# Optimization experiments

Measured on AMD Instinct MI355X. Metric: run time of the kernel, lower is better.

## Reference

```python
import jax, jax.numpy as jnp
import numpy as np

EMB_DIM, TREE_DIM, OUT_DIM, VOCAB = 256, 256, 3, 10000
T, B, LEVELS = 255, 128, 8  # complete binary tree of depth 8, 128 trees per input


def _build_forest():
    # node j = T-1-heap(j): root (heap 0) is the LAST node so stack_last_h picks the root.
    heap = np.arange(T)
    depth = np.floor(np.log2(heap + 1)).astype(np.int64)  # 0..7
    node_order = np.empty(T, dtype=np.int64)
    node_order[T - 1 - heap] = (LEVELS - 1) - depth       # leaves=0, root=7
    internal = np.arange((T - 1) // 2)                     # heaps with two children
    parent = np.repeat(T - 1 - internal, 2)
    child = np.stack([T - 1 - (2 * internal + 1), T - 1 - (2 * internal + 2)], 1).reshape(-1)
    edges = np.stack([parent, child], axis=1)              # (254, 2)
    edge_order = node_order[parent]
    offs = (np.arange(B) * T)[:, None, None]
    adj = (edges[None] + offs).reshape(-1, 2)              # (B*254, 2)
    return np.tile(node_order, B), adj, np.tile(edge_order, B)


def setup_inputs() -> dict:
    key = jax.random.key(0)
    ks = jax.random.split(key, 16)
    no, adj, eo = _build_forest()
    D = TREE_DIM
    s_e = 1.0 / np.sqrt(EMB_DIM)
    s_t = 1.0 / np.sqrt(D)
    return {
        'feat_cube': jax.random.randint(ks[0], (B * T,), 0, VOCAB),
        'feat_a': jax.random.randint(ks[1], (B * T,), 0, VOCAB),
        'feat_b': jax.random.randint(ks[2], (B * T,), 0, VOCAB),
        'node_order': jnp.asarray(no),
        'adjacency_list': jnp.asarray(adj),
        'edge_order': jnp.asarray(eo),
        'num_levels': LEVELS,
        'num_trees': B,
        'emb': jax.random.normal(ks[3], (VOCAB, EMB_DIM), jnp.float32),
        'W_iou': jax.random.normal(ks[4], (3 * D, EMB_DIM), jnp.float32) * s_e,
        'b_iou': jnp.zeros((3 * D,), jnp.float32),
        'U_iou': jax.random.normal(ks[5], (3 * D, D), jnp.float32) * s_t,
        'W_f': jax.random.normal(ks[6], (D, EMB_DIM), jnp.float32) * s_e,
        'b_f': jnp.zeros((D,), jnp.float32),
        'U_f': jax.random.normal(ks[7], (D, D), jnp.float32) * s_t,
        'fc1_w': jax.random.normal(ks[8], (D // 2, D), jnp.float32) * s_t,
        'fc1_b': jnp.zeros((D // 2,), jnp.float32),
        'fc2_w': jax.random.normal(ks[9], (OUT_DIM, D // 2), jnp.float32) * (1.0 / np.sqrt(D // 2)),
        'fc2_b': jnp.zeros((OUT_DIM,), jnp.float32),
    }


def _tree_lstm(x, node_order, parents, children, edge_order, W_iou, b_iou, U_iou, W_f, b_f, U_f, num_levels):
    # Child-sum TreeLSTM, evaluated level by level (leaves first). Dense masked
    # formulation: per level we update only nodes with node_order==lvl; edge
    # contributions are masked before segment_sum (same math as the torch loop).
    N = x.shape[0]
    D = U_f.shape[0]
    x_iou = x @ W_iou.T + b_iou            # (N, 3D), precomputed once
    x_f = x @ W_f.T + b_f                  # (N, D)
    h = jnp.zeros((N, D), x.dtype)
    c = jnp.zeros((N, D), x.dtype)
    for lvl in range(num_levels):
        emask = (edge_order == lvl)[:, None].astype(x.dtype)
        ch = h[children]                   # (E, D) gather of child hidden
        cc = c[children]
        f = jax.nn.sigmoid(x_f[parents] + ch @ U_f.T)
        h_sum = jax.ops.segment_sum(ch * emask, parents, num_segments=N)
        c_sum = jax.ops.segment_sum(f * cc * emask, parents, num_segments=N)
        i, o, u = jnp.split(x_iou + h_sum @ U_iou.T, 3, axis=1)
        c_new = jax.nn.sigmoid(i) * jnp.tanh(u) + c_sum
        h_new = jax.nn.sigmoid(o) * jnp.tanh(c_new)
        nmask = (node_order == lvl)[:, None]
        h = jnp.where(nmask, h_new, h)
        c = jnp.where(nmask, c_new, c)
    return h, c


def reference(feat_cube, feat_a, feat_b, node_order, adjacency_list, edge_order,
              num_levels, num_trees, emb, W_iou, b_iou, U_iou, W_f, b_f, U_f,
              fc1_w, fc1_b, fc2_w, fc2_b):
    parents = adjacency_list[:, 0]
    children = adjacency_list[:, 1]

    def run_tree(feat):
        h, _ = _tree_lstm(emb[feat], node_order, parents, children, edge_order,
                          W_iou, b_iou, U_iou, W_f, b_f, U_f, num_levels)
        # stack_last_h: last node of each tree (= root with our labeling)
        return h.reshape(num_trees, -1, h.shape[-1])[:, -1, :]

    h_c = run_tree(feat_cube)
    h_a = run_tree(feat_a)
    h_b = run_tree(feat_b)
    # h_c (1,D) @ (h_a (D,1) @ h_b (1,D)) == (h_c . h_a) * h_b, fused einsum
    h = jnp.einsum('bi,bi,bj->bj', h_c, h_a, h_b)
    hid = jax.nn.relu(h @ fc1_w.T + fc1_b)
    logits = jax.nn.relu(hid @ fc2_w.T + fc2_b)
    return logits  # (num_trees, out_dim)
```

## Files before the change

### kernel.cpp

```cpp
#include <hip/hip_runtime.h>
#include <hip/hip_bf16.h>

typedef __hip_bfloat16 bf16;
typedef unsigned short u16;
typedef __attribute__((ext_vector_type(8))) short s8;
typedef __attribute__((ext_vector_type(4))) float f4;

#define NRUNS 3
#define NTREE 128
#define TT    255
#define DD    256
#define VPAD  10016
#define PAD   258
#define ESTR  776

__device__ __forceinline__ float bits2f(u16 b){ union{unsigned u; float f;} x; x.u = ((unsigned)b)<<16; return x.f; }
__device__ __forceinline__ u16   f2bits(float f){ bf16 h = __float2bfloat16(f); return *(u16*)&h; }
__device__ __forceinline__ float sigm(float x){ return 1.f/(1.f+__expf(-x)); }
__device__ __forceinline__ float tanh_(float x){ return 1.f - 2.f/(__expf(2.f*x)+1.f); }

__global__ void k_detect(const u16* __restrict__ raw, int* __restrict__ flag){
    int t = threadIdx.x;
    int hit = 0;
    if (t < 128){
        u16 w = raw[2*t];
        int e = (w >> 7) & 0xFF;
        hit = (e >= 100 && e <= 141) ? 1 : 0;
    }
    __shared__ int cnt;
    if (t == 0) cnt = 0;
    __syncthreads();
    atomicAdd(&cnt, hit);
    __syncthreads();
    if (t == 0) flag[0] = (cnt >= 64) ? 1 : 0;
}

__device__ __forceinline__ u16 cvt1b(const void* p, int i, int isb){
    return isb ? ((const u16*)p)[i] : f2bits(((const float*)p)[i]);
}
__device__ __forceinline__ float cvt1f(const void* p, int i, int isb){
    return isb ? bits2f(((const u16*)p)[i]) : ((const float*)p)[i];
}

#define L_EMB  (10000*256)
#define L_EMBP (VPAD*256)
#define L_WIOU (768*256)
#define L_UIOU (768*256)
#define L_WF   (256*256)
#define L_UF   (256*256)
#define L_ALL  (L_EMBP + L_WIOU + L_UIOU + L_WF + L_UF)
__global__ void k_cvtb(const void* __restrict__ s0, const void* __restrict__ s1,
                       const void* __restrict__ s2, const void* __restrict__ s3,
                       const void* __restrict__ s4,
                       u16* __restrict__ d0, u16* __restrict__ d1, u16* __restrict__ d2,
                       u16* __restrict__ d3, u16* __restrict__ d4,
                       const int* __restrict__ flag){
    int isb = flag[0];
    for (int i = blockIdx.x*blockDim.x + threadIdx.x; i < L_ALL; i += gridDim.x*blockDim.x){
        int j = i;
        if (j < L_EMBP){ d0[j] = (j < L_EMB) ? cvt1b(s0, j, isb) : (u16)0; continue; } j -= L_EMBP;
        if (j < L_WIOU){ d1[j] = cvt1b(s1, j, isb); continue; } j -= L_WIOU;
        if (j < L_UIOU){ d2[j] = cvt1b(s2, j, isb); continue; } j -= L_UIOU;
        if (j < L_WF){ d3[j] = cvt1b(s3, j, isb); continue; } j -= L_WF;
        d4[j] = cvt1b(s4, j, isb);
    }
}

#define S_BIOU 768
#define S_BF   256
#define S_F1W  (128*256)
#define S_F1B  128
#define S_F2W  (3*128)
#define S_F2B  3
#define S_ALL  (S_BIOU+S_BF+S_F1W+S_F1B+S_F2W+S_F2B)
__global__ void k_small(const void* __restrict__ s0, const void* __restrict__ s1,
                        const void* __restrict__ s2, const void* __restrict__ s3,
                        const void* __restrict__ s4, const void* __restrict__ s5,
                        float* __restrict__ d0, float* __restrict__ d1, float* __restrict__ d2,
                        float* __restrict__ d3, float* __restrict__ d4, float* __restrict__ d5,
                        const int* __restrict__ flag){
    int isb = flag[0];
    for (int i = blockIdx.x*blockDim.x + threadIdx.x; i < S_ALL; i += gridDim.x*blockDim.x){
        int j = i;
        if (j < S_BIOU){ d0[j] = cvt1f(s0, j, isb); continue; } j -= S_BIOU;
        if (j < S_BF){ d1[j] = cvt1f(s1, j, isb); continue; } j -= S_BF;
        if (j < S_F1W){ d2[j] = cvt1f(s2, j, isb); continue; } j -= S_F1W;
        if (j < S_F1B){ d3[j] = cvt1f(s3, j, isb); continue; } j -= S_F1B;
        if (j < S_F2W){ d4[j] = cvt1f(s4, j, isb); continue; } j -= S_F2W;
        d5[j] = cvt1f(s5, j, isb);
    }
}

__device__ __forceinline__ s8 ldB16(const u16* p){
    union { uint4 q; s8 v; } u;
    u.q = *(const uint4*)p;
    return u.v;
}
__device__ __forceinline__ s8 ldsA(const u16* p){
    union { unsigned w[4]; s8 v; } u;
    u.w[0] = *(const unsigned*)(p);
    u.w[1] = *(const unsigned*)(p+2);
    u.w[2] = *(const unsigned*)(p+4);
    u.w[3] = *(const unsigned*)(p+6);
    return u.v;
}
#define MFMA(acc,a,b) acc = __builtin_amdgcn_mfma_f32_16x16x32_bf16(a, b, acc, 0, 0, 0)

__global__ __launch_bounds__(512, 4)
void k_vocab2(const u16* __restrict__ embb,
              const u16* __restrict__ Wiou, const u16* __restrict__ Wfm,
              const u16* __restrict__ Ufm,  const float* __restrict__ biou_f,
              u16* __restrict__ E_iou, u16* __restrict__ E_f,
              u16* __restrict__ H0, u16* __restrict__ C0, u16* __restrict__ HU0)
{
    __shared__ u16 hs[32*PAD];
    const int t = threadIdx.x, w = t>>6, lane = t&63, ln = lane&15, q = lane>>4;
    const int r0 = blockIdx.x*32, d0 = w*32;

    const u16* Bp[8];
    #pragma unroll
    for (int g = 0; g < 4; g++)
      #pragma unroll
      for (int nc = 0; nc < 2; nc++){
        int nn = d0 + nc*16 + ln;
        Bp[g*2+nc] = (g < 3) ? (Wiou + (size_t)(g*256+nn)*DD) : (Wfm + (size_t)nn*DD);
      }
    const u16* a0p = embb + (size_t)(r0+ln)*DD;
    const u16* a1p = embb + (size_t)(r0+16+ln)*DD;
    f4 acc[8][2];
    #pragma unroll
    for (int nt = 0; nt < 8; nt++){ acc[nt][0] = (f4){0,0,0,0}; acc[nt][1] = (f4){0,0,0,0}; }
    #pragma unroll 2
    for (int ks = 0; ks < 8; ks++){
        int ko = ks*32 + q*8;
        s8 a0 = ldB16(a0p + ko);
        s8 a1 = ldB16(a1p + ko);
        #pragma unroll
        for (int nt = 0; nt < 8; nt++){
            s8 bb = ldB16(Bp[nt] + ko);
            MFMA(acc[nt][0], a0, bb);
            MFMA(acc[nt][1], a1, bb);
        }
    }
    #pragma unroll
    for (int nc = 0; nc < 2; nc++){
        int d = d0 + nc*16 + ln;
        float bi = biou_f[d], bo = biou_f[256+d], bu = biou_f[512+d];
        #pragma unroll
        for (int ms = 0; ms < 2; ms++)
          #pragma unroll
          for (int r = 0; r < 4; r++){
            int vrow = r0 + ms*16 + q*4 + r;
            float ei = acc[0*2+nc][ms][r];
            float eo = acc[1*2+nc][ms][r];
            float eu = acc[2*2+nc][ms][r];
            float ef = acc[3*2+nc][ms][r];
            size_t eb = (size_t)vrow*768 + d;
            E_iou[eb]       = f2bits(ei);
            E_iou[eb + 256] = f2bits(eo);
            E_iou[eb + 512] = f2bits(eu);
            E_f[(size_t)vrow*DD + d] = f2bits(ef);
            float cc = sigm(ei + bi)*tanh_(eu + bu);
            float hh = sigm(eo + bo)*tanh_(cc);
            C0[(size_t)vrow*DD + d] = f2bits(cc);
            H0[(size_t)vrow*DD + d] = f2bits(hh);
            hs[(ms*16 + q*4 + r)*PAD + d] = f2bits(hh);
        }
    }
    __syncthreads();

    f4 hacc[2][2];
    #pragma unroll
    for (int nt = 0; nt < 2; nt++){ hacc[nt][0] = (f4){0,0,0,0}; hacc[nt][1] = (f4){0,0,0,0}; }
    const u16* Bf0 = Ufm + (size_t)(d0 + ln)*DD;
    const u16* Bf1 = Ufm + (size_t)(d0 + 16 + ln)*DD;
    #pragma unroll 2
    for (int ks = 0; ks < 8; ks++){
        int ko = ks*32 + q*8;
        s8 a0 = ldsA(&hs[ln*PAD + ko]);
        s8 a1 = ldsA(&hs[(16+ln)*PAD + ko]);
        s8 b0 = ldB16(Bf0 + ko);
        s8 b1 = ldB16(Bf1 + ko);
        MFMA(hacc[0][0], a0, b0); MFMA(hacc[0][1], a1, b0);
        MFMA(hacc[1][0], a0, b1); MFMA(hacc[1][1], a1, b1);
    }
    #pragma unroll
    for (int nc = 0; nc < 2; nc++){
        int d = d0 + nc*16 + ln;
        #pragma unroll
        for (int ms = 0; ms < 2; ms++)
          #pragma unroll
          for (int r = 0; r < 4; r++){
            int vrow = r0 + ms*16 + q*4 + r;
            HU0[(size_t)vrow*DD + d] = f2bits(hacc[nc][ms][r]);
        }
    }
}

__global__ __launch_bounds__(512, 4)
void k_edge0(const int* __restrict__ f0, const int* __restrict__ f1, const int* __restrict__ f2,
             const u16* __restrict__ E_f, const u16* __restrict__ H0,
             const u16* __restrict__ C0,  const u16* __restrict__ HU0,
             const float* __restrict__ bf_f,
             u16* __restrict__ hsum_out, u16* __restrict__ fcsum_out)
{
    int gid = blockIdx.x*512 + threadIdx.x;
    int row = gid >> 5, ch = gid & 31, d = ch*8;
    int run = row >> 13, rem = row & 8191, b = rem >> 6, jj = rem & 63;
    const int* fp = (run==0) ? f0 : ((run==1) ? f1 : f2);
    int fo = fp[b*TT + 128 + jj];
    int v1 = fp[b*TT + 2*jj];
    int v2 = fp[b*TT + 2*jj + 1];
    s8 ef  = ldB16(E_f + (size_t)fo*DD + d);
    s8 hu1 = ldB16(HU0 + (size_t)v1*DD + d);
    s8 hu2 = ldB16(HU0 + (size_t)v2*DD + d);
    s8 c1  = ldB16(C0  + (size_t)v1*DD + d);
    s8 c2  = ldB16(C0  + (size_t)v2*DD + d);
    s8 h1  = ldB16(H0  + (size_t)v1*DD + d);
    s8 h2  = ldB16(H0  + (size_t)v2*DD + d);
    union { u16 a[8]; uint4 q4; } uh, uf;
    #pragma unroll
    for (int j = 0; j < 8; j++){
        float e  = bits2f((u16)ef[j]) + bf_f[d+j];
        float fa = sigm(e + bits2f((u16)hu1[j]));
        float fb = sigm(e + bits2f((u16)hu2[j]));
        float fc = fa*bits2f((u16)c1[j]) + fb*bits2f((u16)c2[j]);
        float hsv = bits2f((u16)h1[j]) + bits2f((u16)h2[j]);
        uf.a[j] = f2bits(fc);
        uh.a[j] = f2bits(hsv);
    }
    *(uint4*)(hsum_out  + (size_t)row*DD + d) = uh.q4;
    *(uint4*)(fcsum_out + (size_t)row*DD + d) = uf.q4;
}

__global__ __launch_bounds__(512, 4)
void k_lvl(int lvl, int cLog,
           const int* __restrict__ f0, const int* __restrict__ f1, const int* __restrict__ f2,
           const u16* __restrict__ E_iou, const u16* __restrict__ E_f,
           const u16* __restrict__ Uiou, const u16* __restrict__ Ufm,
           const float* __restrict__ biou_f, const float* __restrict__ bf_f,
           const u16* __restrict__ hsum_in, const u16* __restrict__ fcsum_in,
           u16* __restrict__ hsum_out, u16* __restrict__ fcsum_out,
           u16* __restrict__ hroot)
{
    __shared__ u16 es[32*ESTR];
    __shared__ u16 hs[32*PAD];
    const int t = threadIdx.x, w = t>>6, lane = t&63, ln = lane&15, q = lane>>4;
    const int cnt = 1 << cLog, S = 256 - 2*cnt;
    const int r0 = blockIdx.x*32, d0 = w*32;
    const bool haveP = (lvl < 7);

    uint4 stg[6];
    {
        int srow = t >> 4, c16 = t & 15;
        int rho = r0 + srow;
        int run = rho >> (7+cLog);
        int rem = rho & ((1<<(7+cLog)) - 1);
        int b = rem >> cLog, jj = rem & (cnt-1);
        const int* fp = (run==0) ? f0 : ((run==1) ? f1 : f2);
        int feat_s = fp[b*TT + S + jj];
        const u16* ep = E_iou + (size_t)feat_s*768;
        #pragma unroll
        for (int it = 0; it < 6; it++){
            int chk = it*16 + c16;
            stg[it] = *(const uint4*)(ep + chk*8);
        }
    }

    int featp[2][2];
    if (haveP){
        #pragma unroll
        for (int ms = 0; ms < 2; ms++)
          #pragma unroll
          for (int rr = 0; rr < 2; rr++){
            int rho = r0 + ms*16 + q*4 + rr*2;
            int run = rho >> (7+cLog);
            int rem = rho & ((1<<(7+cLog)) - 1);
            int b = rem >> cLog, jj = rem & (cnt-1);
            const int* fp = (run==0) ? f0 : ((run==1) ? f1 : f2);
            featp[ms][rr] = fp[b*TT + (256-cnt) + (jj>>1)];
          }
    }

    f4 acc[6][2];
    #pragma unroll
    for (int nt = 0; nt < 6; nt++){ acc[nt][0] = (f4){0,0,0,0}; acc[nt][1] = (f4){0,0,0,0}; }
    {
        const u16* a0p = hsum_in + (size_t)(r0+ln)*DD;
        const u16* a1p = hsum_in + (size_t)(r0+16+ln)*DD;
        const u16* Bp[6];
        #pragma unroll
        for (int nt = 0; nt < 6; nt++){
            int n = (nt>>1)*256 + d0 + (nt&1)*16 + ln;
            Bp[nt] = Uiou + (size_t)n*DD;
        }
        #pragma unroll 2
        for (int ks = 0; ks < 8; ks++){
            int ko = ks*32 + q*8;
            s8 a0 = ldB16(a0p + ko);
            s8 a1 = ldB16(a1p + ko);
            #pragma unroll
            for (int nt = 0; nt < 6; nt++){
                s8 bb = ldB16(Bp[nt] + ko);
                MFMA(acc[nt][0], a0, bb);
                MFMA(acc[nt][1], a1, bb);
            }
        }
    }

    {
        int srow = t >> 4, c16 = t & 15;
        #pragma unroll
        for (int it = 0; it < 6; it++){
            int chk = it*16 + c16;
            *(uint4*)&es[srow*ESTR + chk*8] = stg[it];
        }
    }
    __syncthreads();

    float cv[2][2][4];
    #pragma unroll
    for (int nc = 0; nc < 2; nc++){
        int d = d0 + nc*16 + ln;
        float bi = biou_f[d], bo = biou_f[256+d], bu = biou_f[512+d];
        #pragma unroll
        for (int ms = 0; ms < 2; ms++){
            float hv[4];
            #pragma unroll
            for (int r = 0; r < 4; r++){
                int m   = ms*16 + q*4 + r;
                int rho = r0 + m;
                float iv = acc[0+nc][ms][r] + bits2f(es[m*ESTR + d])       + bi;
                float ov = acc[2+nc][ms][r] + bits2f(es[m*ESTR + 256 + d]) + bo;
                float uv = acc[4+nc][ms][r] + bits2f(es[m*ESTR + 512 + d]) + bu;
                float cs = bits2f(fcsum_in[(size_t)rho*DD + d]);
                float c = sigm(iv)*tanh_(uv) + cs;
                float h = sigm(ov)*tanh_(c);
                cv[nc][ms][r] = c;
                hv[r] = h;
                if (haveP) hs[m*PAD + d] = f2bits(h);
                else       hroot[(size_t)rho*DD + d] = f2bits(h);
            }
            if (haveP){
                int prow = (r0>>1) + ms*8 + q*2;
                hsum_out[(size_t)prow*DD + d]     = f2bits(hv[0] + hv[1]);
                hsum_out[(size_t)(prow+1)*DD + d] = f2bits(hv[2] + hv[3]);
            }
        }
    }

    if (haveP){
        __syncthreads();
        f4 hacc[2][2];
        #pragma unroll
        for (int nt = 0; nt < 2; nt++){ hacc[nt][0] = (f4){0,0,0,0}; hacc[nt][1] = (f4){0,0,0,0}; }
        const u16* Bf0 = Ufm + (size_t)(d0 + ln)*DD;
        const u16* Bf1 = Ufm + (size_t)(d0 + 16 + ln)*DD;
        #pragma unroll 2
        for (int ks = 0; ks < 8; ks++){
            int ko = ks*32 + q*8;
            s8 a0 = ldsA(&hs[ln*PAD + ko]);
            s8 a1 = ldsA(&hs[(16+ln)*PAD + ko]);
            s8 b0 = ldB16(Bf0 + ko);
            s8 b1 = ldB16(Bf1 + ko);
            MFMA(hacc[0][0], a0, b0); MFMA(hacc[0][1], a1, b0);
            MFMA(hacc[1][0], a0, b1); MFMA(hacc[1][1], a1, b1);
        }
        #pragma unroll
        for (int nc = 0; nc < 2; nc++){
            int d = d0 + nc*16 + ln;
            float bfv = bf_f[d];
            #pragma unroll
            for (int ms = 0; ms < 2; ms++){
                float fs0, fs1;
                #pragma unroll
                for (int r = 0; r < 4; r++){
                    float ef = bits2f(E_f[(size_t)featp[ms][r>>1]*DD + d]);
                    float fc = sigm(ef + bfv + hacc[nc][ms][r]) * cv[nc][ms][r];
                    if (r == 0) fs0 = fc;
                    else if (r == 1) fs0 += fc;
                    else if (r == 2) fs1 = fc;
                    else fs1 += fc;
                }
                int prow = (r0>>1) + ms*8 + q*2;
                fcsum_out[(size_t)prow*DD + d]     = f2bits(fs0);
                fcsum_out[(size_t)(prow+1)*DD + d] = f2bits(fs1);
            }
        }
    }
}

__global__ __launch_bounds__(256)
void k_final(const u16* __restrict__ hroot,
             const float* __restrict__ fc1w, const float* __restrict__ fc1b,
             const float* __restrict__ fc2w, const float* __restrict__ fc2b,
             void* __restrict__ out, const int* __restrict__ flag)
{
    int b = blockIdx.x, t = threadIdx.x;
    __shared__ float sprod[DD];
    __shared__ float shb[DD];
    __shared__ float shid[128];
    float hc  = bits2f(hroot[(0*NTREE + b)*DD + t]);
    float ha  = bits2f(hroot[(1*NTREE + b)*DD + t]);
    float hbv = bits2f(hroot[(2*NTREE + b)*DD + t]);
    sprod[t] = hc * ha;
    shb[t]   = hbv;
    __syncthreads();
    for (int s = 128; s > 0; s >>= 1){
        if (t < s) sprod[t] += sprod[t + s];
        __syncthreads();
    }
    float dot = sprod[0];
    if (t < 128){
        float acc = fc1b[t];
        for (int k = 0; k < DD; k++)
            acc = fmaf(dot * shb[k], fc1w[t*DD + k], acc);
        shid[t] = fmaxf(acc, 0.f);
    }
    __syncthreads();
    if (t < 3){
        float acc = fc2b[t];
        for (int j = 0; j < 128; j++)
            acc = fmaf(fc2w[t*128 + j], shid[j], acc);
        float v = fmaxf(acc, 0.f);
        if (flag[0]) ((bf16*)out)[b*3 + t] = __float2bfloat16(v);
        else         ((float*)out)[b*3 + t] = v;
    }
}

extern "C" void kernel_launch(void* const* d_in, const int* in_sizes, int n_in,
                              void* d_out, int out_size, void* d_ws, size_t ws_size,
                              hipStream_t stream)
{
    const int* f0 = (const int*)d_in[0];
    const int* f1 = (const int*)d_in[1];
    const int* f2 = (const int*)d_in[2];
    const void* emb  = d_in[8];
    const void* Wiou = d_in[9];
    const void* biou = d_in[10];
    const void* Uiou = d_in[11];
    const void* Wf   = d_in[12];
    const void* bfv  = d_in[13];
    const void* Uf   = d_in[14];
    const void* fc1w = d_in[15];
    const void* fc1b = d_in[16];
    const void* fc2w = d_in[17];
    const void* fc2b = d_in[18];

    char* base = (char*)d_ws;
    size_t off = 0;
    auto take = [&](size_t bytes) -> char* {
        char* p = base + off;
        off = (off + bytes + 255) & ~(size_t)255;
        return p;
    };
    int*   flag   = (int*)  take(256);
    u16*   embb   = (u16*)  take((size_t)L_EMBP*2);
    u16*   wioub  = (u16*)  take((size_t)L_WIOU*2);
    u16*   uioub  = (u16*)  take((size_t)L_UIOU*2);
    u16*   wfb    = (u16*)  take((size_t)L_WF*2);
    u16*   ufb    = (u16*)  take((size_t)L_UF*2);
    float* biou_f = (float*)take(S_BIOU*4);
    float* bf_f   = (float*)take(S_BF*4);
    float* fc1w_f = (float*)take(S_F1W*4);
    float* fc1b_f = (float*)take(S_F1B*4);
    float* fc2w_f = (float*)take(S_F2W*4);
    float* fc2b_f = (float*)take(S_F2B*4);
    u16*   E_iou  = (u16*)  take((size_t)VPAD*768*2);
    u16*   E_f    = (u16*)  take((size_t)VPAD*DD*2);
    u16*   H0     = (u16*)  take((size_t)VPAD*DD*2);
    u16*   C0     = (u16*)  take((size_t)VPAD*DD*2);
    u16*   HU0    = (u16*)  take((size_t)VPAD*DD*2);
    u16*   HA     = (u16*)  take((size_t)24576*DD*2);
    u16*   HB     = (u16*)  take((size_t)12288*DD*2);
    u16*   FA     = (u16*)  take((size_t)24576*DD*2);
    u16*   FB     = (u16*)  take((size_t)12288*DD*2);
    u16*   hroot  = (u16*)  take((size_t)NRUNS*NTREE*DD*2);

    k_detect<<<1, 256, 0, stream>>>((const u16*)emb, flag);
    k_cvtb<<<2048, 256, 0, stream>>>(emb, Wiou, Uiou, Wf, Uf,
                                     embb, wioub, uioub, wfb, ufb, flag);
    k_small<<<135, 256, 0, stream>>>(biou, bfv, fc1w, fc1b, fc2w, fc2b,
                                     biou_f, bf_f, fc1w_f, fc1b_f, fc2w_f, fc2b_f, flag);
    k_vocab2<<<VPAD/32, 512, 0, stream>>>(embb, wioub, wfb, ufb, biou_f,
                                          E_iou, E_f, H0, C0, HU0);
    k_edge0<<<24576*32/512, 512, 0, stream>>>(f0, f1, f2, E_f, H0, C0, HU0, bf_f, HA, FA);

    for (int lvl = 1; lvl <= 7; lvl++){
        int cLog = 7 - lvl;
        int rows = NRUNS*NTREE*(128 >> lvl);
        int blocks = rows / 32;
        int pe = lvl & 1;
        u16* hs_o = pe ? HB : HA;
        u16* fc_o = pe ? FB : FA;
        const u16* hs_i = pe ? HA : HB;
        const u16* fc_i = pe ? FA : FB;
        k_lvl<<<blocks, 512, 0, stream>>>(lvl, cLog, f0, f1, f2,
                                          E_iou, E_f, uioub, ufb,
                                          biou_f, bf_f,
                                          hs_i, fc_i, hs_o, fc_o, hroot);
    }
    k_final<<<NTREE, 256, 0, stream>>>(hroot, fc1w_f, fc1b_f, fc2w_f, fc2b_f, d_out, flag);
}
```

Baseline: 438.9 us.

## Fuse level-0 edge aggregation into level-1 kernel and merge conversion kernels

Replaces the separate level-0 edge kernel and level-1 pass with one kernel, k_lvl1. It computes the child h-sum matmul directly as two MFMA accumulations over the gathered leaf rows, and computes the forget-gate cell sums inline. This removes the round trip of the large HA/FA intermediates through global memory and one launch. It also merges the two dtype-conversion kernels into one launch. Separately, it drops the LDS staging of the E_iou rows in k_lvl, which now reads them directly from global memory per element. That makes the reads scattered and uncoalesced, which could hurt.

```diff
diff --git a/kernel.cpp b/kernel.cpp
--- a/kernel.cpp
+++ b/kernel.cpp
@@ -12,7 +12,6 @@
 #define DD    256
 #define VPAD  10016
 #define PAD   258
-#define ESTR  776
 
 __device__ __forceinline__ float bits2f(u16 b){ union{unsigned u; float f;} x; x.u = ((unsigned)b)<<16; return x.f; }
 __device__ __forceinline__ u16   f2bits(float f){ bf16 h = __float2bfloat16(f); return *(u16*)&h; }
@@ -49,23 +48,6 @@
 #define L_WF   (256*256)
 #define L_UF   (256*256)
 #define L_ALL  (L_EMBP + L_WIOU + L_UIOU + L_WF + L_UF)
-__global__ void k_cvtb(const void* __restrict__ s0, const void* __restrict__ s1,
-                       const void* __restrict__ s2, const void* __restrict__ s3,
-                       const void* __restrict__ s4,
-                       u16* __restrict__ d0, u16* __restrict__ d1, u16* __restrict__ d2,
-                       u16* __restrict__ d3, u16* __restrict__ d4,
-                       const int* __restrict__ flag){
-    int isb = flag[0];
-    for (int i = blockIdx.x*blockDim.x + threadIdx.x; i < L_ALL; i += gridDim.x*blockDim.x){
-        int j = i;
-        if (j < L_EMBP){ d0[j] = (j < L_EMB) ? cvt1b(s0, j, isb) : (u16)0; continue; } j -= L_EMBP;
-        if (j < L_WIOU){ d1[j] = cvt1b(s1, j, isb); continue; } j -= L_WIOU;
-        if (j < L_UIOU){ d2[j] = cvt1b(s2, j, isb); continue; } j -= L_UIOU;
-        if (j < L_WF){ d3[j] = cvt1b(s3, j, isb); continue; } j -= L_WF;
-        d4[j] = cvt1b(s4, j, isb);
-    }
-}
-
 #define S_BIOU 768
 #define S_BF   256
 #define S_F1W  (128*256)
@@ -73,21 +55,31 @@
 #define S_F2W  (3*128)
 #define S_F2B  3
 #define S_ALL  (S_BIOU+S_BF+S_F1W+S_F1B+S_F2W+S_F2B)
-__global__ void k_small(const void* __restrict__ s0, const void* __restrict__ s1,
-                        const void* __restrict__ s2, const void* __restrict__ s3,
-                        const void* __restrict__ s4, const void* __restrict__ s5,
-                        float* __restrict__ d0, float* __restrict__ d1, float* __restrict__ d2,
-                        float* __restrict__ d3, float* __restrict__ d4, float* __restrict__ d5,
-                        const int* __restrict__ flag){
+__global__ void k_cvtall(const void* __restrict__ s0, const void* __restrict__ s1,
+                         const void* __restrict__ s2, const void* __restrict__ s3,
+                         const void* __restrict__ s4,
+                         const void* __restrict__ t0, const void* __restrict__ t1,
+                         const void* __restrict__ t2, const void* __restrict__ t3,
+                         const void* __restrict__ t4, const void* __restrict__ t5,
+                         u16* __restrict__ d0, u16* __restrict__ d1, u16* __restrict__ d2,
+                         u16* __restrict__ d3, u16* __restrict__ d4,
+                         float* __restrict__ e0, float* __restrict__ e1, float* __restrict__ e2,
+                         float* __restrict__ e3, float* __restrict__ e4, float* __restrict__ e5,
+                         const int* __restrict__ flag){
     int isb = flag[0];
-    for (int i = blockIdx.x*blockDim.x + threadIdx.x; i < S_ALL; i += gridDim.x*blockDim.x){
+    for (int i = blockIdx.x*blockDim.x + threadIdx.x; i < L_ALL + S_ALL; i += gridDim.x*blockDim.x){
         int j = i;
-        if (j < S_BIOU){ d0[j] = cvt1f(s0, j, isb); continue; } j -= S_BIOU;
-        if (j < S_BF){ d1[j] = cvt1f(s1, j, isb); continue; } j -= S_BF;
-        if (j < S_F1W){ d2[j] = cvt1f(s2, j, isb); continue; } j -= S_F1W;
-        if (j < S_F1B){ d3[j] = cvt1f(s3, j, isb); continue; } j -= S_F1B;
-        if (j < S_F2W){ d4[j] = cvt1f(s4, j, isb); continue; } j -= S_F2W;
-        d5[j] = cvt1f(s5, j, isb);
+        if (j < L_EMBP){ d0[j] = (j < L_EMB) ? cvt1b(s0, j, isb) : (u16)0; continue; } j -= L_EMBP;
+        if (j < L_WIOU){ d1[j] = cvt1b(s1, j, isb); continue; } j -= L_WIOU;
+        if (j < L_UIOU){ d2[j] = cvt1b(s2, j, isb); continue; } j -= L_UIOU;
+        if (j < L_WF){ d3[j] = cvt1b(s3, j, isb); continue; } j -= L_WF;
+        if (j < L_UF){ d4[j] = cvt1b(s4, j, isb); continue; } j -= L_UF;
+        if (j < S_BIOU){ e0[j] = cvt1f(t0, j, isb); continue; } j -= S_BIOU;
+        if (j < S_BF){ e1[j] = cvt1f(t1, j, isb); continue; } j -= S_BF;
+        if (j < S_F1W){ e2[j] = cvt1f(t2, j, isb); continue; } j -= S_F1W;
+        if (j < S_F1B){ e3[j] = cvt1f(t3, j, isb); continue; } j -= S_F1B;
+        if (j < S_F2W){ e4[j] = cvt1f(t4, j, isb); continue; } j -= S_F2W;
+        e5[j] = cvt1f(t5, j, isb);
     }
 }
 
@@ -198,39 +190,140 @@
 }
 
 __global__ __launch_bounds__(512, 4)
-void k_edge0(const int* __restrict__ f0, const int* __restrict__ f1, const int* __restrict__ f2,
-             const u16* __restrict__ E_f, const u16* __restrict__ H0,
-             const u16* __restrict__ C0,  const u16* __restrict__ HU0,
-             const float* __restrict__ bf_f,
-             u16* __restrict__ hsum_out, u16* __restrict__ fcsum_out)
+void k_lvl1(const int* __restrict__ f0, const int* __restrict__ f1, const int* __restrict__ f2,
+            const u16* __restrict__ E_iou, const u16* __restrict__ E_f,
+            const u16* __restrict__ H0, const u16* __restrict__ C0, const u16* __restrict__ HU0,
+            const u16* __restrict__ Uiou, const u16* __restrict__ Ufm,
+            const float* __restrict__ biou_f, const float* __restrict__ bf_f,
+            u16* __restrict__ hsum_out, u16* __restrict__ fcsum_out)
 {
-    int gid = blockIdx.x*512 + threadIdx.x;
-    int row = gid >> 5, ch = gid & 31, d = ch*8;
-    int run = row >> 13, rem = row & 8191, b = rem >> 6, jj = rem & 63;
-    const int* fp = (run==0) ? f0 : ((run==1) ? f1 : f2);
-    int fo = fp[b*TT + 128 + jj];
-    int v1 = fp[b*TT + 2*jj];
-    int v2 = fp[b*TT + 2*jj + 1];
-    s8 ef  = ldB16(E_f + (size_t)fo*DD + d);
-    s8 hu1 = ldB16(HU0 + (size_t)v1*DD + d);
-    s8 hu2 = ldB16(HU0 + (size_t)v2*DD + d);
-    s8 c1  = ldB16(C0  + (size_t)v1*DD + d);
-    s8 c2  = ldB16(C0  + (size_t)v2*DD + d);
-    s8 h1  = ldB16(H0  + (size_t)v1*DD + d);
-    s8 h2  = ldB16(H0  + (size_t)v2*DD + d);
-    union { u16 a[8]; uint4 q4; } uh, uf;
-    #pragma unroll
-    for (int j = 0; j < 8; j++){
-        float e  = bits2f((u16)ef[j]) + bf_f[d+j];
-        float fa = sigm(e + bits2f((u16)hu1[j]));
-        float fb = sigm(e + bits2f((u16)hu2[j]));
-        float fc = fa*bits2f((u16)c1[j]) + fb*bits2f((u16)c2[j]);
-        float hsv = bits2f((u16)h1[j]) + bits2f((u16)h2[j]);
-        uf.a[j] = f2bits(fc);
-        uh.a[j] = f2bits(hsv);
-    }
-    *(uint4*)(hsum_out  + (size_t)row*DD + d) = uh.q4;
-    *(uint4*)(fcsum_out + (size_t)row*DD + d) = uf.q4;
+    __shared__ u16 hs[32*PAD];
+    const int t = threadIdx.x, w = t>>6, lane = t&63, ln = lane&15, q = lane>>4;
+    const int r0 = blockIdx.x*32, d0 = w*32;
+
+    const u16 *pa1[2], *pa2[2];
+    #pragma unroll
+    for (int ms = 0; ms < 2; ms++){
+        int row = r0 + ms*16 + ln;
+        int run = row >> 13, rem = row & 8191;
+        int b = rem >> 6, jj = rem & 63;
+        const int* fp = (run==0) ? f0 : ((run==1) ? f1 : f2);
+        pa1[ms] = H0 + (size_t)fp[b*TT + 2*jj]*DD;
+        pa2[ms] = H0 + (size_t)fp[b*TT + 2*jj + 1]*DD;
+    }
+    int fo[2][4], v1e[2][4], v2e[2][4], featp[2][2];
+    #pragma unroll
+    for (int ms = 0; ms < 2; ms++)
+      #pragma unroll
+      for (int r = 0; r < 4; r++){
+        int rho = r0 + ms*16 + q*4 + r;
+        int run = rho >> 13, rem = rho & 8191;
+        int b = rem >> 6, jj = rem & 63;
+        const int* fp = (run==0) ? f0 : ((run==1) ? f1 : f2);
+        fo[ms][r]  = fp[b*TT + 128 + jj];
+        v1e[ms][r] = fp[b*TT + 2*jj];
+        v2e[ms][r] = fp[b*TT + 2*jj + 1];
+        if ((r&1)==0) featp[ms][r>>1] = fp[b*TT + 192 + (jj>>1)];
+      }
+
+    f4 acc[6][2];
+    #pragma unroll
+    for (int nt = 0; nt < 6; nt++){ acc[nt][0] = (f4){0,0,0,0}; acc[nt][1] = (f4){0,0,0,0}; }
+    {
+        const u16* Bp[6];
+        #pragma unroll
+        for (int nt = 0; nt < 6; nt++){
+            int n = (nt>>1)*256 + d0 + (nt&1)*16 + ln;
+            Bp[nt] = Uiou + (size_t)n*DD;
+        }
+        #pragma unroll 2
+        for (int ks = 0; ks < 8; ks++){
+            int ko = ks*32 + q*8;
+            s8 a10 = ldB16(pa1[0] + ko);
+            s8 a11 = ldB16(pa1[1] + ko);
+            s8 a20 = ldB16(pa2[0] + ko);
+            s8 a21 = ldB16(pa2[1] + ko);
+            #pragma unroll
+            for (int nt = 0; nt < 6; nt++){
+                s8 bb = ldB16(Bp[nt] + ko);
+                MFMA(acc[nt][0], a10, bb);
+                MFMA(acc[nt][0], a20, bb);
+                MFMA(acc[nt][1], a11, bb);
+                MFMA(acc[nt][1], a21, bb);
+            }
+        }
+    }
+
+    float cv[2][2][4];
+    #pragma unroll
+    for (int nc = 0; nc < 2; nc++){
+        int d = d0 + nc*16 + ln;
+        float bi = biou_f[d], bo = biou_f[256+d], bu = biou_f[512+d];
+        float bfv = bf_f[d];
+        #pragma unroll
+        for (int ms = 0; ms < 2; ms++){
+            float hv[4];
+            #pragma unroll
+            for (int r = 0; r < 4; r++){
+                size_t eb = (size_t)fo[ms][r]*768 + d;
+                float iv = acc[0+nc][ms][r] + bits2f(E_iou[eb])       + bi;
+                float ov = acc[2+nc][ms][r] + bits2f(E_iou[eb + 256]) + bo;
+                float uv = acc[4+nc][ms][r] + bits2f(E_iou[eb + 512]) + bu;
+                float e  = bits2f(E_f[(size_t)fo[ms][r]*DD + d]) + bfv;
+                size_t b1 = (size_t)v1e[ms][r]*DD + d;
+                size_t b2 = (size_t)v2e[ms][r]*DD + d;
+                float fa = sigm(e + bits2f(HU0[b1]));
+                float fb = sigm(e + bits2f(HU0[b2]));
+                float cs = fa*bits2f(C0[b1]) + fb*bits2f(C0[b2]);
+                float c = sigm(iv)*tanh_(uv) + cs;
+                float h = sigm(ov)*tanh_(c);
+                cv[nc][ms][r] = c;
+                hv[r] = h;
+                hs[(ms*16 + q*4 + r)*PAD + d] = f2bits(h);
+            }
+            int prow = (r0>>1) + ms*8 + q*2;
+            hsum_out[(size_t)prow*DD + d]     = f2bits(hv[0] + hv[1]);
+            hsum_out[(size_t)(prow+1)*DD + d] = f2bits(hv[2] + hv[3]);
+        }
+    }
+
+    __syncthreads();
+    f4 hacc[2][2];
+    #pragma unroll
+    for (int nt = 0; nt < 2; nt++){ hacc[nt][0] = (f4){0,0,0,0}; hacc[nt][1] = (f4){0,0,0,0}; }
+    const u16* Bf0 = Ufm + (size_t)(d0 + ln)*DD;
+    const u16* Bf1 = Ufm + (size_t)(d0 + 16 + ln)*DD;
+    #pragma unroll 2
+    for (int ks = 0; ks < 8; ks++){
+        int ko = ks*32 + q*8;
+        s8 a0 = ldsA(&hs[ln*PAD + ko]);
+        s8 a1 = ldsA(&hs[(16+ln)*PAD + ko]);
+        s8 b0 = ldB16(Bf0 + ko);
+        s8 b1 = ldB16(Bf1 + ko);
+        MFMA(hacc[0][0], a0, b0); MFMA(hacc[0][1], a1, b0);
+        MFMA(hacc[1][0], a0, b1); MFMA(hacc[1][1], a1, b1);
+    }
+    #pragma unroll
+    for (int nc = 0; nc < 2; nc++){
+        int d = d0 + nc*16 + ln;
+        float bfv = bf_f[d];
+        #pragma unroll
+        for (int ms = 0; ms < 2; ms++){
+            float fs0, fs1;
+            #pragma unroll
+            for (int r = 0; r < 4; r++){
+                float ef = bits2f(E_f[(size_t)featp[ms][r>>1]*DD + d]);
+                float fc = sigm(ef + bfv + hacc[nc][ms][r]) * cv[nc][ms][r];
+                if (r == 0) fs0 = fc;
+                else if (r == 1) fs0 += fc;
+                else if (r == 2) fs1 = fc;
+                else fs1 += fc;
+            }
+            int prow = (r0>>1) + ms*8 + q*2;
+            fcsum_out[(size_t)prow*DD + d]     = f2bits(fs0);
+            fcsum_out[(size_t)(prow+1)*DD + d] = f2bits(fs1);
+        }
+    }
 }
 
 __global__ __launch_bounds__(512, 4)
@@ -243,44 +336,26 @@
            u16* __restrict__ hsum_out, u16* __restrict__ fcsum_out,
            u16* __restrict__ hroot)
 {
-    __shared__ u16 es[32*ESTR];
     __shared__ u16 hs[32*PAD];
     const int t = threadIdx.x, w = t>>6, lane = t&63, ln = lane&15, q = lane>>4;
     const int cnt = 1 << cLog, S = 256 - 2*cnt;
     const int r0 = blockIdx.x*32, d0 = w*32;
     const bool haveP = (lvl < 7);
 
-    uint4 stg[6];
-    {
-        int srow = t >> 4, c16 = t & 15;
-        int rho = r0 + srow;
+    int feat[2][4], featp[2][2];
+    #pragma unroll
+    for (int ms = 0; ms < 2; ms++)
+      #pragma unroll
+      for (int r = 0; r < 4; r++){
+        int rho = r0 + ms*16 + q*4 + r;
         int run = rho >> (7+cLog);
         int rem = rho & ((1<<(7+cLog)) - 1);
         int b = rem >> cLog, jj = rem & (cnt-1);
         const int* fp = (run==0) ? f0 : ((run==1) ? f1 : f2);
-        int feat_s = fp[b*TT + S + jj];
-        const u16* ep = E_iou + (size_t)feat_s*768;
-        #pragma unroll
-        for (int it = 0; it < 6; it++){
-            int chk = it*16 + c16;
-            stg[it] = *(const uint4*)(ep + chk*8);
-        }
-    }
-
-    int featp[2][2];
-    if (haveP){
-        #pragma unroll
-        for (int ms = 0; ms < 2; ms++)
-          #pragma unroll
-          for (int rr = 0; rr < 2; rr++){
-            int rho = r0 + ms*16 + q*4 + rr*2;
-            int run = rho >> (7+cLog);
-            int rem = rho & ((1<<(7+cLog)) - 1);
-            int b = rem >> cLog, jj = rem & (cnt-1);
-            const int* fp = (run==0) ? f0 : ((run==1) ? f1 : f2);
-            featp[ms][rr] = fp[b*TT + (256-cnt) + (jj>>1)];
-          }
-    }
+        feat[ms][r] = fp[b*TT + S + jj];
+        if (haveP && (r&1)==0)
+            featp[ms][r>>1] = fp[b*TT + (256-cnt) + (jj>>1)];
+      }
 
     f4 acc[6][2];
     #pragma unroll
@@ -308,16 +383,6 @@
         }
     }
 
-    {
-        int srow = t >> 4, c16 = t & 15;
-        #pragma unroll
-        for (int it = 0; it < 6; it++){
-            int chk = it*16 + c16;
-            *(uint4*)&es[srow*ESTR + chk*8] = stg[it];
-        }
-    }
-    __syncthreads();
-
     float cv[2][2][4];
     #pragma unroll
     for (int nc = 0; nc < 2; nc++){
@@ -328,17 +393,17 @@
             float hv[4];
             #pragma unroll
             for (int r = 0; r < 4; r++){
-                int m   = ms*16 + q*4 + r;
-                int rho = r0 + m;
-                float iv = acc[0+nc][ms][r] + bits2f(es[m*ESTR + d])       + bi;
-                float ov = acc[2+nc][ms][r] + bits2f(es[m*ESTR + 256 + d]) + bo;
-                float uv = acc[4+nc][ms][r] + bits2f(es[m*ESTR + 512 + d]) + bu;
+                int rho = r0 + ms*16 + q*4 + r;
+                size_t eb = (size_t)feat[ms][r]*768 + d;
+                float iv = acc[0+nc][ms][r] + bits2f(E_iou[eb])       + bi;
+                float ov = acc[2+nc][ms][r] + bits2f(E_iou[eb + 256]) + bo;
+                float uv = acc[4+nc][ms][r] + bits2f(E_iou[eb + 512]) + bu;
                 float cs = bits2f(fcsum_in[(size_t)rho*DD + d]);
                 float c = sigm(iv)*tanh_(uv) + cs;
                 float h = sigm(ov)*tanh_(c);
                 cv[nc][ms][r] = c;
                 hv[r] = h;
-                if (haveP) hs[m*PAD + d] = f2bits(h);
+                if (haveP) hs[(ms*16 + q*4 + r)*PAD + d] = f2bits(h);
                 else       hroot[(size_t)rho*DD + d] = f2bits(h);
             }
             if (haveP){
@@ -471,22 +536,23 @@
     u16*   H0     = (u16*)  take((size_t)VPAD*DD*2);
     u16*   C0     = (u16*)  take((size_t)VPAD*DD*2);
     u16*   HU0    = (u16*)  take((size_t)VPAD*DD*2);
-    u16*   HA     = (u16*)  take((size_t)24576*DD*2);
     u16*   HB     = (u16*)  take((size_t)12288*DD*2);
-    u16*   FA     = (u16*)  take((size_t)24576*DD*2);
     u16*   FB     = (u16*)  take((size_t)12288*DD*2);
+    u16*   HA     = (u16*)  take((size_t)6144*DD*2);
+    u16*   FA     = (u16*)  take((size_t)6144*DD*2);
     u16*   hroot  = (u16*)  take((size_t)NRUNS*NTREE*DD*2);
 
     k_detect<<<1, 256, 0, stream>>>((const u16*)emb, flag);
-    k_cvtb<<<2048, 256, 0, stream>>>(emb, Wiou, Uiou, Wf, Uf,
-                                     embb, wioub, uioub, wfb, ufb, flag);
-    k_small<<<135, 256, 0, stream>>>(biou, bfv, fc1w, fc1b, fc2w, fc2b,
-                                     biou_f, bf_f, fc1w_f, fc1b_f, fc2w_f, fc2b_f, flag);
+    k_cvtall<<<2048, 256, 0, stream>>>(emb, Wiou, Uiou, Wf, Uf,
+                                       biou, bfv, fc1w, fc1b, fc2w, fc2b,
+                                       embb, wioub, uioub, wfb, ufb,
+                                       biou_f, bf_f, fc1w_f, fc1b_f, fc2w_f, fc2b_f, flag);
     k_vocab2<<<VPAD/32, 512, 0, stream>>>(embb, wioub, wfb, ufb, biou_f,
                                           E_iou, E_f, H0, C0, HU0);
-    k_edge0<<<24576*32/512, 512, 0, stream>>>(f0, f1, f2, E_f, H0, C0, HU0, bf_f, HA, FA);
-
-    for (int lvl = 1; lvl <= 7; lvl++){
+    k_lvl1<<<768, 512, 0, stream>>>(f0, f1, f2, E_iou, E_f, H0, C0, HU0,
+                                    uioub, ufb, biou_f, bf_f, HB, FB);
+
+    for (int lvl = 2; lvl <= 7; lvl++){
         int cLog = 7 - lvl;
         int rows = NRUNS*NTREE*(128 >> lvl);
         int blocks = rows / 32;
```

Measured after the change: 472.1 us. +7.6%, slower.

## Merge conversion kernels and read embedding projections directly instead of staging through LDS

Applied to the files above, without the earlier changes.

Fuses the bf16 weight conversion and the small fp32 parameter conversion into one kernel, removing a launch. In the level kernel, the E_iou rows are no longer staged into a large shared buffer with a block barrier. Each thread now gathers its own i/o/u elements straight from global memory in the epilogue. This cuts LDS usage, which may raise occupancy, and removes a sync, but it trades coalesced 16-byte staging loads for scattered 2-byte global reads. Buffer allocation order is also shuffled.

```diff
diff --git a/kernel.cpp b/kernel.cpp
--- a/kernel.cpp
+++ b/kernel.cpp
@@ -12,7 +12,6 @@
 #define DD    256
 #define VPAD  10016
 #define PAD   258
-#define ESTR  776
 
 __device__ __forceinline__ float bits2f(u16 b){ union{unsigned u; float f;} x; x.u = ((unsigned)b)<<16; return x.f; }
 __device__ __forceinline__ u16   f2bits(float f){ bf16 h = __float2bfloat16(f); return *(u16*)&h; }
@@ -49,23 +48,6 @@
 #define L_WF   (256*256)
 #define L_UF   (256*256)
 #define L_ALL  (L_EMBP + L_WIOU + L_UIOU + L_WF + L_UF)
-__global__ void k_cvtb(const void* __restrict__ s0, const void* __restrict__ s1,
-                       const void* __restrict__ s2, const void* __restrict__ s3,
-                       const void* __restrict__ s4,
-                       u16* __restrict__ d0, u16* __restrict__ d1, u16* __restrict__ d2,
-                       u16* __restrict__ d3, u16* __restrict__ d4,
-                       const int* __restrict__ flag){
-    int isb = flag[0];
-    for (int i = blockIdx.x*blockDim.x + threadIdx.x; i < L_ALL; i += gridDim.x*blockDim.x){
-        int j = i;
-        if (j < L_EMBP){ d0[j] = (j < L_EMB) ? cvt1b(s0, j, isb) : (u16)0; continue; } j -= L_EMBP;
-        if (j < L_WIOU){ d1[j] = cvt1b(s1, j, isb); continue; } j -= L_WIOU;
-        if (j < L_UIOU){ d2[j] = cvt1b(s2, j, isb); continue; } j -= L_UIOU;
-        if (j < L_WF){ d3[j] = cvt1b(s3, j, isb); continue; } j -= L_WF;
-        d4[j] = cvt1b(s4, j, isb);
-    }
-}
-
 #define S_BIOU 768
 #define S_BF   256
 #define S_F1W  (128*256)
@@ -73,21 +55,31 @@
 #define S_F2W  (3*128)
 #define S_F2B  3
 #define S_ALL  (S_BIOU+S_BF+S_F1W+S_F1B+S_F2W+S_F2B)
-__global__ void k_small(const void* __restrict__ s0, const void* __restrict__ s1,
-                        const void* __restrict__ s2, const void* __restrict__ s3,
-                        const void* __restrict__ s4, const void* __restrict__ s5,
-                        float* __restrict__ d0, float* __restrict__ d1, float* __restrict__ d2,
-                        float* __restrict__ d3, float* __restrict__ d4, float* __restrict__ d5,
-                        const int* __restrict__ flag){
+__global__ void k_cvtall(const void* __restrict__ s0, const void* __restrict__ s1,
+                         const void* __restrict__ s2, const void* __restrict__ s3,
+                         const void* __restrict__ s4,
+                         const void* __restrict__ t0, const void* __restrict__ t1,
+                         const void* __restrict__ t2, const void* __restrict__ t3,
+                         const void* __restrict__ t4, const void* __restrict__ t5,
+                         u16* __restrict__ d0, u16* __restrict__ d1, u16* __restrict__ d2,
+                         u16* __restrict__ d3, u16* __restrict__ d4,
+                         float* __restrict__ e0, float* __restrict__ e1, float* __restrict__ e2,
+                         float* __restrict__ e3, float* __restrict__ e4, float* __restrict__ e5,
+                         const int* __restrict__ flag){
     int isb = flag[0];
-    for (int i = blockIdx.x*blockDim.x + threadIdx.x; i < S_ALL; i += gridDim.x*blockDim.x){
+    for (int i = blockIdx.x*blockDim.x + threadIdx.x; i < L_ALL + S_ALL; i += gridDim.x*blockDim.x){
         int j = i;
-        if (j < S_BIOU){ d0[j] = cvt1f(s0, j, isb); continue; } j -= S_BIOU;
-        if (j < S_BF){ d1[j] = cvt1f(s1, j, isb); continue; } j -= S_BF;
-        if (j < S_F1W){ d2[j] = cvt1f(s2, j, isb); continue; } j -= S_F1W;
-        if (j < S_F1B){ d3[j] = cvt1f(s3, j, isb); continue; } j -= S_F1B;
-        if (j < S_F2W){ d4[j] = cvt1f(s4, j, isb); continue; } j -= S_F2W;
-        d5[j] = cvt1f(s5, j, isb);
+        if (j < L_EMBP){ d0[j] = (j < L_EMB) ? cvt1b(s0, j, isb) : (u16)0; continue; } j -= L_EMBP;
+        if (j < L_WIOU){ d1[j] = cvt1b(s1, j, isb); continue; } j -= L_WIOU;
+        if (j < L_UIOU){ d2[j] = cvt1b(s2, j, isb); continue; } j -= L_UIOU;
+        if (j < L_WF){ d3[j] = cvt1b(s3, j, isb); continue; } j -= L_WF;
+        if (j < L_UF){ d4[j] = cvt1b(s4, j, isb); continue; } j -= L_UF;
+        if (j < S_BIOU){ e0[j] = cvt1f(t0, j, isb); continue; } j -= S_BIOU;
+        if (j < S_BF){ e1[j] = cvt1f(t1, j, isb); continue; } j -= S_BF;
+        if (j < S_F1W){ e2[j] = cvt1f(t2, j, isb); continue; } j -= S_F1W;
+        if (j < S_F1B){ e3[j] = cvt1f(t3, j, isb); continue; } j -= S_F1B;
+        if (j < S_F2W){ e4[j] = cvt1f(t4, j, isb); continue; } j -= S_F2W;
+        e5[j] = cvt1f(t5, j, isb);
     }
 }
 
@@ -243,44 +235,26 @@
            u16* __restrict__ hsum_out, u16* __restrict__ fcsum_out,
            u16* __restrict__ hroot)
 {
-    __shared__ u16 es[32*ESTR];
     __shared__ u16 hs[32*PAD];
     const int t = threadIdx.x, w = t>>6, lane = t&63, ln = lane&15, q = lane>>4;
     const int cnt = 1 << cLog, S = 256 - 2*cnt;
     const int r0 = blockIdx.x*32, d0 = w*32;
     const bool haveP = (lvl < 7);
 
-    uint4 stg[6];
-    {
-        int srow = t >> 4, c16 = t & 15;
-        int rho = r0 + srow;
+    int feat[2][4], featp[2][2];
+    #pragma unroll
+    for (int ms = 0; ms < 2; ms++)
+      #pragma unroll
+      for (int r = 0; r < 4; r++){
+        int rho = r0 + ms*16 + q*4 + r;
         int run = rho >> (7+cLog);
         int rem = rho & ((1<<(7+cLog)) - 1);
         int b = rem >> cLog, jj = rem & (cnt-1);
         const int* fp = (run==0) ? f0 : ((run==1) ? f1 : f2);
-        int feat_s = fp[b*TT + S + jj];
-        const u16* ep = E_iou + (size_t)feat_s*768;
-        #pragma unroll
-        for (int it = 0; it < 6; it++){
-            int chk = it*16 + c16;
-            stg[it] = *(const uint4*)(ep + chk*8);
-        }
-    }
-
-    int featp[2][2];
-    if (haveP){
-        #pragma unroll
-        for (int ms = 0; ms < 2; ms++)
-          #pragma unroll
-          for (int rr = 0; rr < 2; rr++){
-            int rho = r0 + ms*16 + q*4 + rr*2;
-            int run = rho >> (7+cLog);
-            int rem = rho & ((1<<(7+cLog)) - 1);
-            int b = rem >> cLog, jj = rem & (cnt-1);
-            const int* fp = (run==0) ? f0 : ((run==1) ? f1 : f2);
-            featp[ms][rr] = fp[b*TT + (256-cnt) + (jj>>1)];
-          }
-    }
+        feat[ms][r] = fp[b*TT + S + jj];
+        if (haveP && (r&1)==0)
+            featp[ms][r>>1] = fp[b*TT + (256-cnt) + (jj>>1)];
+      }
 
     f4 acc[6][2];
     #pragma unroll
@@ -308,16 +282,6 @@
         }
     }
 
-    {
-        int srow = t >> 4, c16 = t & 15;
-        #pragma unroll
-        for (int it = 0; it < 6; it++){
-            int chk = it*16 + c16;
-            *(uint4*)&es[srow*ESTR + chk*8] = stg[it];
-        }
-    }
-    __syncthreads();
-
     float cv[2][2][4];
     #pragma unroll
     for (int nc = 0; nc < 2; nc++){
@@ -328,17 +292,17 @@
             float hv[4];
             #pragma unroll
             for (int r = 0; r < 4; r++){
-                int m   = ms*16 + q*4 + r;
-                int rho = r0 + m;
-                float iv = acc[0+nc][ms][r] + bits2f(es[m*ESTR + d])       + bi;
-                float ov = acc[2+nc][ms][r] + bits2f(es[m*ESTR + 256 + d]) + bo;
-                float uv = acc[4+nc][ms][r] + bits2f(es[m*ESTR + 512 + d]) + bu;
+                int rho = r0 + ms*16 + q*4 + r;
+                size_t eb = (size_t)feat[ms][r]*768 + d;
+                float iv = acc[0+nc][ms][r] + bits2f(E_iou[eb])       + bi;
+                float ov = acc[2+nc][ms][r] + bits2f(E_iou[eb + 256]) + bo;
+                float uv = acc[4+nc][ms][r] + bits2f(E_iou[eb + 512]) + bu;
                 float cs = bits2f(fcsum_in[(size_t)rho*DD + d]);
                 float c = sigm(iv)*tanh_(uv) + cs;
                 float h = sigm(ov)*tanh_(c);
                 cv[nc][ms][r] = c;
                 hv[r] = h;
-                if (haveP) hs[m*PAD + d] = f2bits(h);
+                if (haveP) hs[(ms*16 + q*4 + r)*PAD + d] = f2bits(h);
                 else       hroot[(size_t)rho*DD + d] = f2bits(h);
             }
             if (haveP){
@@ -471,17 +435,17 @@
     u16*   H0     = (u16*)  take((size_t)VPAD*DD*2);
     u16*   C0     = (u16*)  take((size_t)VPAD*DD*2);
     u16*   HU0    = (u16*)  take((size_t)VPAD*DD*2);
+    u16*   HB     = (u16*)  take((size_t)12288*DD*2);
+    u16*   FB     = (u16*)  take((size_t)12288*DD*2);
     u16*   HA     = (u16*)  take((size_t)24576*DD*2);
-    u16*   HB     = (u16*)  take((size_t)12288*DD*2);
     u16*   FA     = (u16*)  take((size_t)24576*DD*2);
-    u16*   FB     = (u16*)  take((size_t)12288*DD*2);
     u16*   hroot  = (u16*)  take((size_t)NRUNS*NTREE*DD*2);
 
     k_detect<<<1, 256, 0, stream>>>((const u16*)emb, flag);
-    k_cvtb<<<2048, 256, 0, stream>>>(emb, Wiou, Uiou, Wf, Uf,
-                                     embb, wioub, uioub, wfb, ufb, flag);
-    k_small<<<135, 256, 0, stream>>>(biou, bfv, fc1w, fc1b, fc2w, fc2b,
-                                     biou_f, bf_f, fc1w_f, fc1b_f, fc2w_f, fc2b_f, flag);
+    k_cvtall<<<2048, 256, 0, stream>>>(emb, Wiou, Uiou, Wf, Uf,
+                                       biou, bfv, fc1w, fc1b, fc2w, fc2b,
+                                       embb, wioub, uioub, wfb, ufb,
+                                       biou_f, bf_f, fc1w_f, fc1b_f, fc2w_f, fc2b_f, flag);
     k_vocab2<<<VPAD/32, 512, 0, stream>>>(embb, wioub, wfb, ufb, biou_f,
                                           E_iou, E_f, H0, C0, HU0);
     k_edge0<<<24576*32/512, 512, 0, stream>>>(f0, f1, f2, E_f, H0, C0, HU0, bf_f, HA, FA);
```

After: 449.2 us. +2.4%, slower.
